# Kernel optimization log

Hardware: AMD Instinct MI355X
Metric: run time of the kernel (lower is better)

The kernel has to match this reference:

```python
import jax, jax.numpy as jnp
import numpy as np

B, C, H, W, S = 4, 16, 256, 256, 100
OMEGA2 = (0.01 * S) ** 2  # alpha=0.01, n_spixels=100 -> 1.0
EPS = 1e-32


def setup_inputs() -> dict:
    key = jax.random.key(0)
    ks = jax.random.split(key, 7)
    pf = jax.random.normal(ks[0], (B, C, H, W), jnp.float32)
    spf1 = jax.random.normal(ks[1], (B, C, S), jnp.float32)
    spf2 = jax.random.normal(ks[2], (B, C, S), jnp.float32)
    Q1 = jax.random.uniform(ks[3], (B, S, H * W), jnp.float32)
    Q2 = jax.random.uniform(ks[4], (B, S, H * W), jnp.float32)
    w_ds = jax.random.normal(ks[5], (2, C, 3, 3), jnp.float32) * 0.05
    b_ds = jnp.zeros((2,), jnp.float32)
    return {"pf": pf, "spf1": spf1, "spf2": spf2, "Q1": Q1, "Q2": Q2,
            "w_ds": w_ds, "b_ds": b_ds}


def _affinity_pool(pf_flat, spf, Q):
    """merge=True branch: pairwise superpixel affinities, then affinity-weighted
    normalized pixel->superpixel pooling.
    pf_flat: [B,C,N], spf: [B,C,S] (detached), Q: [B,S,N] (detached)."""
    d = spf[:, :, None, :] - spf[:, :, :, None]          # [B,C,S,S]
    rels = jnp.exp(-jnp.sum(d * d, axis=1) / OMEGA2)      # [B,S,S]
    coeffs = jnp.einsum('bst,btn->bsn', rels, Q)          # map_sp2p(rels, Q)
    num = jnp.einsum('bcn,bsn->bcs', pf_flat, coeffs)     # pf @ coeffs^T
    return num / (jnp.sum(coeffs, axis=-1)[:, None, :] + EPS)  # [B,C,S]


def reference(pf, spf1, spf2, Q1, Q2, w_ds, b_ds):
    b, c, h, w = pf.shape
    pf_flat = pf.reshape(b, c, h * w)
    spf1n = _affinity_pool(pf_flat, spf1, Q1)
    spf2n = _affinity_pool(pf_flat, spf2, Q2)
    # map_sp2p: superpixel features back to pixels
    pf1 = jnp.einsum('bcs,bsn->bcn', spf1n, Q1).reshape(b, c, h, w)
    pf2 = jnp.einsum('bcs,bsn->bcn', spf2n, Q2).reshape(b, c, h, w)
    pf_sp = pf1 + pf2
    # conv_ds: Conv3x3(out_ch, 2), no bn/act
    prob_ds = jax.lax.conv_general_dilated(
        pf_sp, w_ds, window_strides=(1, 1), padding='SAME',
        dimension_numbers=('NCHW', 'OIHW', 'NCHW')) + b_ds[None, :, None, None]
    return prob_ds
```

## Files before the change

### kernel.cpp

```cpp
#include <hip/hip_runtime.h>

#define BB 4
#define CC 16
#define HH 256
#define WW 256
#define NN (HH*WW)
#define SS 100
#define EPSV 1e-32f

#define PQ_OFF    0u
#define SPFN_OFF  13600u
#define PFSP_OFF  26400u
#define PPART_OFF PFSP_OFF

typedef _Float16 f16x8 __attribute__((ext_vector_type(8)));
typedef float f32x4 __attribute__((ext_vector_type(4)));
typedef __fp16 h2 __attribute__((ext_vector_type(2)));
typedef __fp16 h4 __attribute__((ext_vector_type(4)));

#define LQROW(i) { int sl_ = (i) * 256 + tid; int r_ = sl_ >> 4; \
    if (r_ > 99) r_ = 99; qo##i = (size_t)r_ * NN + (sl_ & 15) * 4; }

#define LOADQ(ST) { int so_ = (ST) * 64; \
    lq0 = *(const float4*)(Qb + qo0 + so_); \
    lq1 = *(const float4*)(Qb + qo1 + so_); \
    lq2 = *(const float4*)(Qb + qo2 + so_); \
    lq3 = *(const float4*)(Qb + qo3 + so_); \
    lq4 = *(const float4*)(Qb + qo4 + so_); \
    lq5 = *(const float4*)(Qb + qo5 + so_); \
    lq6 = *(const float4*)(Qb + qo6 + so_); \
    lp0 = *(const float4*)(Pb + po0 + so_); }

#define W1(DST, i, R) { int sl_ = (i) * 256 + tid; \
    int w_ = (sl_ >> 4) * 72 + (sl_ & 15) * 4; \
    h2 ha_ = __builtin_amdgcn_cvt_pkrtz(R.x, R.y); \
    h2 hb_ = __builtin_amdgcn_cvt_pkrtz(R.z, R.w); \
    *(h4*)&DST[w_] = __builtin_shufflevector(ha_, hb_, 0, 1, 2, 3); }

#define CVTW(QL, FL) { \
    W1(QL, 0, lq0) W1(QL, 1, lq1) W1(QL, 2, lq2) W1(QL, 3, lq3) \
    W1(QL, 4, lq4) W1(QL, 5, lq5) W1(QL, 6, lq6) W1(FL, 0, lp0) }

#define KSTEP(QL, FL, J) { \
    f16x8 af = *(const f16x8*)&FL[aoff + (J) * 32]; \
    f16x8 b0 = *(const f16x8*)&QL[boff0 + (J) * 32]; \
    f16x8 b1 = *(const f16x8*)&QL[boff1 + (J) * 32]; \
    acc0 = __builtin_amdgcn_mfma_f32_16x16x32_f16(af, b0, acc0, 0, 0, 0); \
    qac0 = __builtin_amdgcn_mfma_f32_16x16x32_f16(ones, b0, qac0, 0, 0, 0); \
    acc1 = __builtin_amdgcn_mfma_f32_16x16x32_f16(af, b1, acc1, 0, 0, 0); \
    qac1 = __builtin_amdgcn_mfma_f32_16x16x32_f16(ones, b1, qac1, 0, 0, 0); }

#define CMP(QL, FL) { KSTEP(QL, FL, 0) KSTEP(QL, FL, 1) }

__global__ __launch_bounds__(256, 2) void k_pass1(const float* __restrict__ pf,
                                                  const float* __restrict__ Q1,
                                                  const float* __restrict__ Q2,
                                                  float* __restrict__ ws) {
    int tid = threadIdx.x, wid = tid >> 6, lane = tid & 63;
    int chunk = blockIdx.x;
    int bq    = blockIdx.y;
    int b = bq >> 1, q = bq & 1;
    int r16 = lane & 15, g4 = lane >> 4;
    int n0 = chunk * 512;

    const float* Qb = (q ? Q2 : Q1) + (size_t)b * SS * NN + n0;
    const float* Pb = pf + (size_t)b * CC * NN + n0;

    __shared__ __align__(16) __fp16 qldsA[112 * 72];
    __shared__ __align__(16) __fp16 qldsB[112 * 72];
    __shared__ __align__(16) __fp16 fldsA[16 * 72];
    __shared__ __align__(16) __fp16 fldsB[16 * 72];

    size_t qo0, qo1, qo2, qo3, qo4, qo5, qo6;
    LQROW(0) LQROW(1) LQROW(2) LQROW(3) LQROW(4) LQROW(5) LQROW(6)
    size_t po0 = (size_t)(tid >> 4) * NN + (tid & 15) * 4;

    int t0 = wid;
    int t1 = (wid < 3) ? wid + 4 : 3;
    int aoff  = r16 * 72 + g4 * 8;
    int boff0 = (t0 * 16 + r16) * 72 + g4 * 8;
    int boff1 = (t1 * 16 + r16) * 72 + g4 * 8;

    f32x4 acc0 = {0.f, 0.f, 0.f, 0.f}, acc1 = {0.f, 0.f, 0.f, 0.f};
    f32x4 qac0 = {0.f, 0.f, 0.f, 0.f}, qac1 = {0.f, 0.f, 0.f, 0.f};
    const f16x8 ones = {1.f16, 1.f16, 1.f16, 1.f16, 1.f16, 1.f16, 1.f16, 1.f16};

    float4 lq0, lq1, lq2, lq3, lq4, lq5, lq6, lp0;

    LOADQ(0) CVTW(qldsA, fldsA) __syncthreads();
    LOADQ(1) CMP(qldsA, fldsA) CVTW(qldsB, fldsB) __syncthreads();
    LOADQ(2) CMP(qldsB, fldsB) CVTW(qldsA, fldsA) __syncthreads();
    LOADQ(3) CMP(qldsA, fldsA) CVTW(qldsB, fldsB) __syncthreads();
    LOADQ(4) CMP(qldsB, fldsB) CVTW(qldsA, fldsA) __syncthreads();
    LOADQ(5) CMP(qldsA, fldsA) CVTW(qldsB, fldsB) __syncthreads();
    LOADQ(6) CMP(qldsB, fldsB) CVTW(qldsA, fldsA) __syncthreads();
    LOADQ(7) CMP(qldsA, fldsA) CVTW(qldsB, fldsB) __syncthreads();
    CMP(qldsB, fldsB)

    float* sout = ws + PPART_OFF + (size_t)(bq * 128 + chunk) * 1700;
    {
        int s0 = t0 * 16 + r16;
        float* o = sout + (size_t)s0 * 17 + g4 * 4;
        o[0] = acc0[0]; o[1] = acc0[1]; o[2] = acc0[2]; o[3] = acc0[3];
        if (lane < 16) sout[(size_t)s0 * 17 + 16] = qac0[0];
    }
    if (wid < 3) {
        int s1 = (wid + 4) * 16 + r16;
        if (s1 < 100) {
            float* o = sout + (size_t)s1 * 17 + g4 * 4;
            o[0] = acc1[0]; o[1] = acc1[1]; o[2] = acc1[2]; o[3] = acc1[3];
            if (lane < 16) sout[(size_t)s1 * 17 + 16] = qac1[0];
        }
    }
}

__global__ __launch_bounds__(256) void k_reduceP(float* __restrict__ ws) {
    int strip = blockIdx.x;
    int bq    = blockIdx.y;
    int idx = strip * 256 + threadIdx.x;
    if (idx < 1700) {
        const float* pp = ws + PPART_OFF + (size_t)bq * 128 * 1700 + idx;
        float a0 = 0.f, a1 = 0.f;
        #pragma unroll 4
        for (int win = 0; win < 128; win += 2) {
            a0 += pp[(size_t)win * 1700];
            a1 += pp[(size_t)(win + 1) * 1700];
        }
        ws[PQ_OFF + (size_t)bq * 1700 + idx] = a0 + a1;
    }
}

__global__ __launch_bounds__(256) void k_finalize(const float* __restrict__ spf1,
                                                  const float* __restrict__ spf2,
                                                  float* __restrict__ ws) {
    int sq = blockIdx.x;
    int bq = blockIdx.y;
    int b = bq >> 1, q = bq & 1;
    __shared__ float sp[CC][SS];
    __shared__ float rl[25][SS + 1];
    __shared__ float Pl[CC * SS];
    __shared__ float qs[SS];
    __shared__ float den[25];
    int tid = threadIdx.x;

    const float* spf = (q ? spf2 : spf1) + (size_t)b * CC * SS;
    for (int i = tid; i < CC * SS; i += 256) sp[i / SS][i % SS] = spf[i];
    const float* pq = ws + PQ_OFF + (size_t)bq * 1700;
    for (int idx = tid; idx < CC * SS; idx += 256) {
        int c = idx / SS, t = idx % SS;
        Pl[idx] = pq[(size_t)t * 17 + c];
    }
    if (tid < SS) qs[tid] = pq[(size_t)tid * 17 + 16];
    __syncthreads();
    for (int i = tid; i < 25 * SS; i += 256) {
        int sl = i / SS, t = i % SS;
        int s = sq * 25 + sl;
        float d2 = 0.f;
        #pragma unroll
        for (int c = 0; c < CC; ++c) {
            float d = sp[c][t] - sp[c][s];
            d2 += d * d;
        }
        rl[sl][t] = expf(-d2);
    }
    __syncthreads();
    if (tid < 25) {
        float a = 0.f;
        for (int t = 0; t < SS; ++t) a += rl[tid][t] * qs[t];
        den[tid] = a + EPSV;
    }
    __syncthreads();
    float* sout = ws + SPFN_OFF + (size_t)bq * SS * CC;
    for (int idx = tid; idx < 25 * CC; idx += 256) {
        int sl = idx / CC, c = idx % CC;
        float a = 0.f;
        for (int t = 0; t < SS; ++t) a += rl[sl][t] * Pl[c * SS + t];
        sout[(size_t)(sq * 25 + sl) * CC + c] = a / den[sl];
    }
}

#define P2STEP(V1, V2, s) { \
    _Pragma("unroll") for (int g = 0; g < 4; ++g) { \
        float4 s1 = *(const float4*)&spl[(0 * SS + (s)) * CC + g * 4]; \
        float4 s2 = *(const float4*)&spl[(SS + (s)) * CC + g * 4]; \
        acc[g*4+0].x += s1.x*V1.x + s2.x*V2.x; \
        acc[g*4+0].y += s1.x*V1.y + s2.x*V2.y; \
        acc[g*4+1].x += s1.y*V1.x + s2.y*V2.x; \
        acc[g*4+1].y += s1.y*V1.y + s2.y*V2.y; \
        acc[g*4+2].x += s1.z*V1.x + s2.z*V2.x; \
        acc[g*4+2].y += s1.z*V1.y + s2.z*V2.y; \
        acc[g*4+3].x += s1.w*V1.x + s2.w*V2.x; \
        acc[g*4+3].y += s1.w*V1.y + s2.w*V2.y; } }

__global__ __launch_bounds__(128) void k_pass2(const float* __restrict__ Q1,
                                               const float* __restrict__ Q2,
                                               float* __restrict__ ws) {
    int blk = blockIdx.x;
    int b   = blockIdx.y;
    __shared__ float spl[2 * SS * CC];
    int tid = threadIdx.x;
    const float* spin = ws + SPFN_OFF + (size_t)b * 2 * SS * CC;
    for (int idx = tid; idx < 2 * SS * CC; idx += 128) spl[idx] = spin[idx];
    __syncthreads();
    int n = blk * 256 + tid * 2;
    const float* q1p = Q1 + (size_t)b * SS * NN + n;
    const float* q2p = Q2 + (size_t)b * SS * NN + n;
    float2 acc[CC];
    #pragma unroll
    for (int c = 0; c < CC; ++c) acc[c] = make_float2(0.f, 0.f);
    float2 A1, A2, B1, B2;
    A1 = *(const float2*)(q1p);
    A2 = *(const float2*)(q2p);
    #pragma unroll 2
    for (int s = 0; s < 98; s += 2) {
        B1 = *(const float2*)(q1p + (size_t)(s + 1) * NN);
        B2 = *(const float2*)(q2p + (size_t)(s + 1) * NN);
        P2STEP(A1, A2, s)
        A1 = *(const float2*)(q1p + (size_t)(s + 2) * NN);
        A2 = *(const float2*)(q2p + (size_t)(s + 2) * NN);
        P2STEP(B1, B2, s + 1)
    }
    B1 = *(const float2*)(q1p + (size_t)99 * NN);
    B2 = *(const float2*)(q2p + (size_t)99 * NN);
    P2STEP(A1, A2, 98)
    P2STEP(B1, B2, 99)
    float* o = ws + PFSP_OFF + (size_t)b * CC * NN + n;
    #pragma unroll
    for (int c = 0; c < CC; ++c)
        *(float2*)(o + (size_t)c * NN) = acc[c];
}

__global__ __launch_bounds__(256) void k_conv(const float* __restrict__ w_ds,
                                              const float* __restrict__ b_ds,
                                              const float* __restrict__ ws,
                                              float* __restrict__ out) {
    int b = blockIdx.y;
    int n = blockIdx.x * 256 + threadIdx.x;
    __shared__ float wl[2][CC][9];
    __shared__ float bl[2];
    for (int i = threadIdx.x; i < 2 * CC * 9; i += 256)
        ((float*)wl)[i] = w_ds[i];
    if (threadIdx.x < 2) bl[threadIdx.x] = b_ds[threadIdx.x];
    __syncthreads();
    int y = n >> 8, x = n & 255;
    const float* base = ws + PFSP_OFF + (size_t)b * CC * NN;
    float a0 = bl[0], a1 = bl[1];
    for (int c = 0; c < CC; ++c) {
        const float* pc = base + (size_t)c * NN;
        #pragma unroll
        for (int dy = -1; dy <= 1; ++dy) {
            int yy = y + dy;
            if (yy < 0 || yy >= HH) continue;
            #pragma unroll
            for (int dx = -1; dx <= 1; ++dx) {
                int xx = x + dx;
                if (xx < 0 || xx >= WW) continue;
                float v = pc[(size_t)yy * WW + xx];
                int k = (dy + 1) * 3 + (dx + 1);
                a0 += v * wl[0][c][k];
                a1 += v * wl[1][c][k];
            }
        }
    }
    out[((size_t)b * 2 + 0) * NN + n] = a0;
    out[((size_t)b * 2 + 1) * NN + n] = a1;
}

extern "C" void kernel_launch(void* const* d_in, const int* in_sizes, int n_in,
                              void* d_out, int out_size, void* d_ws, size_t ws_size,
                              hipStream_t stream) {
    const float* pf   = (const float*)d_in[0];
    const float* spf1 = (const float*)d_in[1];
    const float* spf2 = (const float*)d_in[2];
    const float* Q1   = (const float*)d_in[3];
    const float* Q2   = (const float*)d_in[4];
    const float* w_ds = (const float*)d_in[5];
    const float* b_ds = (const float*)d_in[6];
    float* ws  = (float*)d_ws;
    float* out = (float*)d_out;

    k_pass1<<<dim3(128, 8), 256, 0, stream>>>(pf, Q1, Q2, ws);
    k_reduceP<<<dim3(7, 8), 256, 0, stream>>>(ws);
    k_finalize<<<dim3(4, 8), 256, 0, stream>>>(spf1, spf2, ws);
    k_pass2<<<dim3(256, BB), 128, 0, stream>>>(Q1, Q2, ws);
    k_conv<<<dim3(NN / 256, BB), 256, 0, stream>>>(w_ds, b_ds, ws, out);
}
```

Measured before the change: 138.8 us.

## Stream Q and pf tiles straight into LDS with global_load_lds and swizzle

The pass-1 pooling kernel used to load Q and pf tiles into registers, convert them to fp16 and write them to padded LDS buffers. It now uses direct global-to-LDS loads (global_load_lds), keeps the tiles in LDS as fp32 with an XOR swizzle against bank conflicts, and converts to fp16 when building the MFMA operands. The aim is to remove the register round-trip and conversion work from the load path and let the copies overlap the MFMA work of the previous stage. The cost is twice the LDS footprint (64KB per block), which may limit occupancy, plus more LDS read traffic and conversion instructions in the inner loop.

```diff
diff --git a/kernel.cpp b/kernel.cpp
--- a/kernel.cpp
+++ b/kernel.cpp
@@ -15,42 +15,42 @@
 
 typedef _Float16 f16x8 __attribute__((ext_vector_type(8)));
 typedef float f32x4 __attribute__((ext_vector_type(4)));
-typedef __fp16 h2 __attribute__((ext_vector_type(2)));
-typedef __fp16 h4 __attribute__((ext_vector_type(4)));
-
-#define LQROW(i) { int sl_ = (i) * 256 + tid; int r_ = sl_ >> 4; \
-    if (r_ > 99) r_ = 99; qo##i = (size_t)r_ * NN + (sl_ & 15) * 4; }
-
-#define LOADQ(ST) { int so_ = (ST) * 64; \
-    lq0 = *(const float4*)(Qb + qo0 + so_); \
-    lq1 = *(const float4*)(Qb + qo1 + so_); \
-    lq2 = *(const float4*)(Qb + qo2 + so_); \
-    lq3 = *(const float4*)(Qb + qo3 + so_); \
-    lq4 = *(const float4*)(Qb + qo4 + so_); \
-    lq5 = *(const float4*)(Qb + qo5 + so_); \
-    lq6 = *(const float4*)(Qb + qo6 + so_); \
-    lp0 = *(const float4*)(Pb + po0 + so_); }
-
-#define W1(DST, i, R) { int sl_ = (i) * 256 + tid; \
-    int w_ = (sl_ >> 4) * 72 + (sl_ & 15) * 4; \
-    h2 ha_ = __builtin_amdgcn_cvt_pkrtz(R.x, R.y); \
-    h2 hb_ = __builtin_amdgcn_cvt_pkrtz(R.z, R.w); \
-    *(h4*)&DST[w_] = __builtin_shufflevector(ha_, hb_, 0, 1, 2, 3); }
-
-#define CVTW(QL, FL) { \
-    W1(QL, 0, lq0) W1(QL, 1, lq1) W1(QL, 2, lq2) W1(QL, 3, lq3) \
-    W1(QL, 4, lq4) W1(QL, 5, lq5) W1(QL, 6, lq6) W1(FL, 0, lp0) }
-
-#define KSTEP(QL, FL, J) { \
-    f16x8 af = *(const f16x8*)&FL[aoff + (J) * 32]; \
-    f16x8 b0 = *(const f16x8*)&QL[boff0 + (J) * 32]; \
-    f16x8 b1 = *(const f16x8*)&QL[boff1 + (J) * 32]; \
-    acc0 = __builtin_amdgcn_mfma_f32_16x16x32_f16(af, b0, acc0, 0, 0, 0); \
-    qac0 = __builtin_amdgcn_mfma_f32_16x16x32_f16(ones, b0, qac0, 0, 0, 0); \
-    acc1 = __builtin_amdgcn_mfma_f32_16x16x32_f16(af, b1, acc1, 0, 0, 0); \
-    qac1 = __builtin_amdgcn_mfma_f32_16x16x32_f16(ones, b1, qac1, 0, 0, 0); }
-
-#define CMP(QL, FL) { KSTEP(QL, FL, 0) KSTEP(QL, FL, 1) }
+
+__device__ __forceinline__ void gload(const float* g, float* l) {
+    __builtin_amdgcn_global_load_lds(
+        (const __attribute__((address_space(1))) void*)g,
+        (__attribute__((address_space(3))) void*)l, 16, 0, 0);
+}
+
+#define STAGE(ST, QD, PD) { \
+    _Pragma("unroll") \
+    for (int i_ = 0; i_ < 7; ++i_) { \
+        int r0_ = wid * 28 + i_ * 4; \
+        int row_ = r0_ + (lane >> 4); if (row_ > 99) row_ = 99; \
+        int co_ = ((lane & 15) * 4) ^ ((row_ & 7) << 2); \
+        gload(Qb + (size_t)row_ * NN + (ST) * 64 + co_, (QD) + r0_ * 64); \
+    } \
+    { int r0_ = wid * 4; int row_ = r0_ + (lane >> 4); \
+      int co_ = ((lane & 15) * 4) ^ ((row_ & 7) << 2); \
+      gload(Pb + (size_t)row_ * NN + (ST) * 64 + co_, (PD) + r0_ * 64); } }
+
+#define MK8(a, b) {(_Float16)a.x, (_Float16)a.y, (_Float16)a.z, (_Float16)a.w, \
+                   (_Float16)b.x, (_Float16)b.y, (_Float16)b.z, (_Float16)b.w}
+
+#define KSTEP(J) { \
+    float4 a0 = *(const float4*)(pc + arow + (J) * 32 + of0); \
+    float4 a1 = *(const float4*)(pc + arow + (J) * 32 + of1); \
+    f16x8 af = MK8(a0, a1); \
+    float4 b00 = *(const float4*)(qc + brow0 + (J) * 32 + of0); \
+    float4 b01 = *(const float4*)(qc + brow0 + (J) * 32 + of1); \
+    f16x8 bf0 = MK8(b00, b01); \
+    float4 b10 = *(const float4*)(qc + brow1 + (J) * 32 + of0); \
+    float4 b11 = *(const float4*)(qc + brow1 + (J) * 32 + of1); \
+    f16x8 bf1 = MK8(b10, b11); \
+    acc0 = __builtin_amdgcn_mfma_f32_16x16x32_f16(af, bf0, acc0, 0, 0, 0); \
+    qac0 = __builtin_amdgcn_mfma_f32_16x16x32_f16(ones, bf0, qac0, 0, 0, 0); \
+    acc1 = __builtin_amdgcn_mfma_f32_16x16x32_f16(af, bf1, acc1, 0, 0, 0); \
+    qac1 = __builtin_amdgcn_mfma_f32_16x16x32_f16(ones, bf1, qac1, 0, 0, 0); }
 
 __global__ __launch_bounds__(256, 2) void k_pass1(const float* __restrict__ pf,
                                                   const float* __restrict__ Q1,
@@ -66,36 +66,36 @@
     const float* Qb = (q ? Q2 : Q1) + (size_t)b * SS * NN + n0;
     const float* Pb = pf + (size_t)b * CC * NN + n0;
 
-    __shared__ __align__(16) __fp16 qldsA[112 * 72];
-    __shared__ __align__(16) __fp16 qldsB[112 * 72];
-    __shared__ __align__(16) __fp16 fldsA[16 * 72];
-    __shared__ __align__(16) __fp16 fldsB[16 * 72];
-
-    size_t qo0, qo1, qo2, qo3, qo4, qo5, qo6;
-    LQROW(0) LQROW(1) LQROW(2) LQROW(3) LQROW(4) LQROW(5) LQROW(6)
-    size_t po0 = (size_t)(tid >> 4) * NN + (tid & 15) * 4;
+    __shared__ __align__(16) float qbufA[112 * 64];
+    __shared__ __align__(16) float qbufB[112 * 64];
+    __shared__ __align__(16) float pbufA[16 * 64];
+    __shared__ __align__(16) float pbufB[16 * 64];
 
     int t0 = wid;
     int t1 = (wid < 3) ? wid + 4 : 3;
-    int aoff  = r16 * 72 + g4 * 8;
-    int boff0 = (t0 * 16 + r16) * 72 + g4 * 8;
-    int boff1 = (t1 * 16 + r16) * 72 + g4 * 8;
+    int arow  = r16 * 64;
+    int brow0 = (t0 * 16 + r16) * 64;
+    int brow1 = (t1 * 16 + r16) * 64;
+    int sw  = (r16 & 7) << 2;
+    int of0 = (g4 * 8) ^ sw;
+    int of1 = (g4 * 8 + 4) ^ sw;
 
     f32x4 acc0 = {0.f, 0.f, 0.f, 0.f}, acc1 = {0.f, 0.f, 0.f, 0.f};
     f32x4 qac0 = {0.f, 0.f, 0.f, 0.f}, qac1 = {0.f, 0.f, 0.f, 0.f};
     const f16x8 ones = {1.f16, 1.f16, 1.f16, 1.f16, 1.f16, 1.f16, 1.f16, 1.f16};
 
-    float4 lq0, lq1, lq2, lq3, lq4, lq5, lq6, lp0;
-
-    LOADQ(0) CVTW(qldsA, fldsA) __syncthreads();
-    LOADQ(1) CMP(qldsA, fldsA) CVTW(qldsB, fldsB) __syncthreads();
-    LOADQ(2) CMP(qldsB, fldsB) CVTW(qldsA, fldsA) __syncthreads();
-    LOADQ(3) CMP(qldsA, fldsA) CVTW(qldsB, fldsB) __syncthreads();
-    LOADQ(4) CMP(qldsB, fldsB) CVTW(qldsA, fldsA) __syncthreads();
-    LOADQ(5) CMP(qldsA, fldsA) CVTW(qldsB, fldsB) __syncthreads();
-    LOADQ(6) CMP(qldsB, fldsB) CVTW(qldsA, fldsA) __syncthreads();
-    LOADQ(7) CMP(qldsA, fldsA) CVTW(qldsB, fldsB) __syncthreads();
-    CMP(qldsB, fldsB)
+    STAGE(0, qbufA, pbufA)
+    __syncthreads();
+    float* qc = qbufA; float* pc = pbufA;
+    float* qn = qbufB; float* pn = pbufB;
+    for (int st = 0; st < 7; ++st) {
+        STAGE(st + 1, qn, pn)
+        KSTEP(0) KSTEP(1)
+        __syncthreads();
+        float* t = qc; qc = qn; qn = t;
+        t = pc; pc = pn; pn = t;
+    }
+    KSTEP(0) KSTEP(1)
 
     float* sout = ws + PPART_OFF + (size_t)(bq * 128 + chunk) * 1700;
     {
```

Result: slower. 147.7 us (+6.4%).
